# Optimization experiments

Measured on AMD Instinct MI355X. Metric: run time of the kernel, lower is better.

The kernel has to match this reference:

```python
import jax, jax.numpy as jnp
import numpy as np


def setup_inputs() -> dict:
    key = jax.random.key(0)
    k1, k2, k3, k4 = jax.random.split(key, 4)
    B, C, T, H, W = 2, 64, 8, 48, 48
    C2 = C // 2
    x_in = jax.random.normal(k1, (B, C, T, H, W), dtype=jnp.float32)
    # per-time-slice 1x1 conv weights (theta/phi pairs), kaiming-ish scale
    theta_w = jax.random.normal(k2, (T, C2, C), dtype=jnp.float32) / np.sqrt(C)
    phi_w = jax.random.normal(k3, (T, C2, C), dtype=jnp.float32) / np.sqrt(C)
    out_w = jax.random.normal(k4, (C, C), dtype=jnp.float32) / np.sqrt(C)
    return {"x_in": x_in, "theta_w": theta_w, "phi_w": phi_w, "out_w": out_w}


def reference(x_in, theta_w, phi_w, out_w):
    B, C, T, H, W = x_in.shape
    C2 = theta_w.shape[1]
    P = H * W
    # [B, T, C, P] layout: flatten spatial, move time next to batch
    x = jnp.transpose(x_in, (0, 2, 1, 3, 4)).reshape(B, T, C, P)
    # per-slice 1x1 convs == per-slice channel matmuls with slice-specific weights
    theta = jnp.einsum("toc,btcp->btop", theta_w, x)  # [B,T,C2,P]
    phi = jnp.einsum("toc,btcp->btop", phi_w, x)      # [B,T,C2,P]
    scale = 1.0 / jnp.sqrt(jnp.asarray(C2, dtype=x_in.dtype))
    scores = jnp.einsum("btcp,btcq->btpq", theta, phi) * scale  # [B,T,P,P]
    attn = jax.nn.softmax(scores, axis=-1)
    f = jnp.einsum("btpq,btcq->btcp", attn, x)  # value = raw x, [B,T,C,P]
    # conv_out: 1x1x1 Conv3d (pointwise over channels), then residual
    out = jnp.einsum("oc,btcp->btop", out_w, f)
    out = jnp.transpose(out.reshape(B, T, C, H, W), (0, 2, 1, 3, 4))
    return out + x_in
```

## Files before the change

kernel.cpp:

```cpp
#include <hip/hip_runtime.h>
#include <hip/hip_bf16.h>

#define CC 64
#define TT 8
#define PP 2304
#define C2 32
#define BT 16
#define NKT 36
#define HKT 18
#define SCALE2 0.25503486f

using h8 = __attribute__((ext_vector_type(8))) _Float16;
using h4 = __attribute__((ext_vector_type(4))) _Float16;
using f4 = __attribute__((ext_vector_type(4))) float;

#if __has_builtin(__builtin_amdgcn_exp2f)
#define EXP2(v) __builtin_amdgcn_exp2f(v)
#else
#define EXP2(v) exp2f(v)
#endif

#define SWIZ_BT(xcd, g) ((xcd) + 8 * ((g) & 1))
#define SWIZ_PT(g) ((g) >> 1)


__global__ __launch_bounds__(256) void k_prep(
    const float* __restrict__ x, const float* __restrict__ tw,
    const float* __restrict__ pw, _Float16* __restrict__ thf,
    _Float16* __restrict__ rec) {
  const int qt = SWIZ_PT(blockIdx.y), bt = SWIZ_BT(blockIdx.x, blockIdx.y);
  const int b = bt >> 3, t = bt & 7;
  const int tid = threadIdx.x;
  const int wv = tid >> 6, lane = tid & 63;
  const int quad = lane >> 4, l15 = lane & 15;

  __shared__ __align__(16) float x_s[64][68];
  __shared__ __align__(16) _Float16 th_s[4][16][32];
  __shared__ __align__(16) _Float16 ph_s[4][16][32];

  const size_t xslice = ((size_t)b * CC * TT + t) * PP;
  const int qg0 = qt * 64;

  {
    const int qq = tid & 63;
    const int c0 = (tid >> 6) * 16;
#pragma unroll
    for (int i = 0; i < 16; i++) {
      int c = c0 + i;
      x_s[qq][c] = x[xslice + (size_t)c * (TT * PP) + qg0 + qq];
    }
  }
  __syncthreads();

  h8 bx[2];
#pragma unroll
  for (int ks = 0; ks < 2; ks++) {
    const float* row = &x_s[wv * 16 + l15][ks * 32 + quad * 8];
    float4 u0 = *reinterpret_cast<const float4*>(row);
    float4 u1 = *reinterpret_cast<const float4*>(row + 4);
    bx[ks][0] = (_Float16)u0.x; bx[ks][1] = (_Float16)u0.y;
    bx[ks][2] = (_Float16)u0.z; bx[ks][3] = (_Float16)u0.w;
    bx[ks][4] = (_Float16)u1.x; bx[ks][5] = (_Float16)u1.y;
    bx[ks][6] = (_Float16)u1.z; bx[ks][7] = (_Float16)u1.w;
  }

  const float* twt = tw + t * C2 * CC;
  const float* pwt = pw + t * C2 * CC;
  const f4 zero = {0.f, 0.f, 0.f, 0.f};
  f4 accT[2] = {zero, zero}, accP[2] = {zero, zero};
#pragma unroll
  for (int mt = 0; mt < 2; mt++)
#pragma unroll
    for (int ks = 0; ks < 2; ks++) {
      const float* wr = twt + (mt * 16 + l15) * CC + ks * 32 + quad * 8;
      const float* pr = pwt + (mt * 16 + l15) * CC + ks * 32 + quad * 8;
      float4 a0 = *reinterpret_cast<const float4*>(wr);
      float4 a1 = *reinterpret_cast<const float4*>(wr + 4);
      float4 p0 = *reinterpret_cast<const float4*>(pr);
      float4 p1 = *reinterpret_cast<const float4*>(pr + 4);
      h8 at = {(_Float16)a0.x, (_Float16)a0.y, (_Float16)a0.z, (_Float16)a0.w,
               (_Float16)a1.x, (_Float16)a1.y, (_Float16)a1.z, (_Float16)a1.w};
      h8 ap = {(_Float16)p0.x, (_Float16)p0.y, (_Float16)p0.z, (_Float16)p0.w,
               (_Float16)p1.x, (_Float16)p1.y, (_Float16)p1.z, (_Float16)p1.w};
      accT[mt] =
          __builtin_amdgcn_mfma_f32_16x16x32_f16(at, bx[ks], accT[mt], 0, 0, 0);
      accP[mt] =
          __builtin_amdgcn_mfma_f32_16x16x32_f16(ap, bx[ks], accP[mt], 0, 0, 0);
    }

#pragma unroll
  for (int mt = 0; mt < 2; mt++) {
    h4 tv, pv;
#pragma unroll
    for (int r = 0; r < 4; r++) {
      tv[r] = (_Float16)(accT[mt][r] * SCALE2);
      pv[r] = (_Float16)accP[mt][r];
    }
    *reinterpret_cast<h4*>(&th_s[wv][l15][mt * 16 + quad * 4]) = tv;
    *reinterpret_cast<h4*>(&ph_s[wv][l15][mt * 16 + quad * 4]) = pv;
  }

  h8 tfrag = *reinterpret_cast<const h8*>(&th_s[wv][l15][quad * 8]);
  *reinterpret_cast<h8*>(
      thf + (((size_t)(bt * NKT + qt) * 4 + wv) * 64 + lane) * 8) = tfrag;

  _Float16* rb = rec + (size_t)(bt * NKT + qt) * 6144;
  h8 pfrag = *reinterpret_cast<const h8*>(&ph_s[wv][l15][quad * 8]);
  *reinterpret_cast<h8*>(rb + wv * 512 + lane * 8) = pfrag;

#pragma unroll
  for (int ctp = 0; ctp < 2; ctp++) {
    h8 v;
#pragma unroll
    for (int j = 0; j < 4; j++) {
      v[j] = (_Float16)x_s[wv * 16 + quad * 4 + j][(2 * ctp) * 16 + l15];
      v[4 + j] = (_Float16)x_s[wv * 16 + quad * 4 + j][(2 * ctp + 1) * 16 + l15];
    }
    *reinterpret_cast<h8*>(rb + 2048 + (wv * 2 + ctp) * 512 + lane * 8) = v;
  }
}

__global__ __launch_bounds__(512, 4) void k_attn(
    const float* __restrict__ x, const _Float16* __restrict__ thf,
    const _Float16* __restrict__ rec, const float* __restrict__ ow,
    float* __restrict__ out) {
  const int pt = SWIZ_PT(blockIdx.y), bt = SWIZ_BT(blockIdx.x, blockIdx.y);
  const int b = bt >> 3, t = bt & 7;
  const int tid = threadIdx.x;
  const int wv = tid >> 6, lane = tid & 63;
  const int quad = lane >> 4, l15 = lane & 15;
  const int qg = wv & 3, kg = wv >> 2;

  __shared__ __align__(16) char smem[49152];
  _Float16* stage = reinterpret_cast<_Float16*>(smem);
  float* exch = reinterpret_cast<float*>(smem);
  float* out_s = reinterpret_cast<float*>(smem + 20480);

  const h8 b_th = *reinterpret_cast<const h8*>(
      thf + (((size_t)(bt * NKT + pt) * 4 + qg) * 64 + lane) * 8);

  const _Float16* recb = rec + (size_t)bt * NKT * 6144;

  const int m0 = wv * 3;
  int ch_tile[3], ch_off[3];
#pragma unroll
  for (int j = 0; j < 3; j++) {
    int m = m0 + j;
    ch_tile[j] = m / 12;
    ch_off[j] = (m % 12) * 512 + lane * 8;
  }

  int4 v[3];
#pragma unroll
  for (int j = 0; j < 3; j++) {
    v[j] = *reinterpret_cast<const int4*>(recb +
                                          (size_t)(ch_tile[j] * HKT) * 6144 +
                                          ch_off[j]);
    *reinterpret_cast<int4*>(stage + ch_tile[j] * 6144 + ch_off[j]) = v[j];
  }

  const f4 zero = {0.f, 0.f, 0.f, 0.f};
  f4 O[4] = {zero, zero, zero, zero};
  float l_sum = 0.f;

  for (int i = 0; i < HKT; i++) {
    __syncthreads();
    const _Float16* cur = stage + (i & 1) * 12288 + kg * 6144;

    if (i < HKT - 1) {
#pragma unroll
      for (int j = 0; j < 3; j++)
        v[j] = *reinterpret_cast<const int4*>(
            recb + (size_t)(ch_tile[j] * HKT + i + 1) * 6144 + ch_off[j]);
    }

    h8 aphi[4];
#pragma unroll
    for (int nt = 0; nt < 4; nt++)
      aphi[nt] = *reinterpret_cast<const h8*>(cur + nt * 512 + lane * 8);
    f4 s[4];
#pragma unroll
    for (int nt = 0; nt < 4; nt++)
      s[nt] =
          __builtin_amdgcn_mfma_f32_16x16x32_f16(aphi[nt], b_th, zero, 0, 0, 0);

#pragma unroll
    for (int nt = 0; nt < 4; nt++) {
      h4 bw;
#pragma unroll
      for (int r = 0; r < 4; r++) {
        float w = EXP2(s[nt][r]);
        l_sum += w;
        bw[r] = (_Float16)w;
      }
#pragma unroll
      for (int ctp = 0; ctp < 2; ctp++) {
        h8 xx = *reinterpret_cast<const h8*>(cur + 2048 +
                                             (nt * 2 + ctp) * 512 + lane * 8);
        h4 a0 = __builtin_shufflevector(xx, xx, 0, 1, 2, 3);
        h4 a1 = __builtin_shufflevector(xx, xx, 4, 5, 6, 7);
        O[2 * ctp] =
            __builtin_amdgcn_mfma_f32_16x16x16f16(a0, bw, O[2 * ctp], 0, 0, 0);
        O[2 * ctp + 1] = __builtin_amdgcn_mfma_f32_16x16x16f16(
            a1, bw, O[2 * ctp + 1], 0, 0, 0);
      }
    }

    if (i < HKT - 1) {
#pragma unroll
      for (int j = 0; j < 3; j++)
        *reinterpret_cast<int4*>(stage + ((i + 1) & 1) * 12288 +
                                 ch_tile[j] * 6144 + ch_off[j]) = v[j];
    }
  }

  l_sum += __shfl_xor(l_sum, 16);
  l_sum += __shfl_xor(l_sum, 32);

  __syncthreads();

  if (kg == 1) {
#pragma unroll
    for (int k = 0; k < 16; k++)
      exch[(qg * 17 + k) * 64 + lane] = O[k >> 2][k & 3];
    exch[(qg * 17 + 16) * 64 + lane] = l_sum;
  }
  __syncthreads();

  if (kg == 0) {
#pragma unroll
    for (int k = 0; k < 16; k++)
      O[k >> 2][k & 3] += exch[(qg * 17 + k) * 64 + lane];
    const float inv = 1.f / (l_sum + exch[(qg * 17 + 16) * 64 + lane]);

    h4 bf[4];
#pragma unroll
    for (int ct = 0; ct < 4; ct++)
#pragma unroll
      for (int r = 0; r < 4; r++) bf[ct][r] = (_Float16)(O[ct][r] * inv);

    f4 D3[4] = {zero, zero, zero, zero};
#pragma unroll
    for (int mt = 0; mt < 4; mt++)
#pragma unroll
      for (int ct = 0; ct < 4; ct++) {
        const float* wrow =
            ow + (size_t)(mt * 16 + l15) * CC + ct * 16 + quad * 4;
        float4 u = *reinterpret_cast<const float4*>(wrow);
        h4 aw = {(_Float16)u.x, (_Float16)u.y, (_Float16)u.z, (_Float16)u.w};
        D3[mt] =
            __builtin_amdgcn_mfma_f32_16x16x16f16(aw, bf[ct], D3[mt], 0, 0, 0);
      }

#pragma unroll
    for (int mt = 0; mt < 4; mt++)
#pragma unroll
      for (int r = 0; r < 4; r++)
        out_s[(mt * 16 + quad * 4 + r) * 68 + qg * 16 + l15] = D3[mt][r];
  }
  __syncthreads();

  const int co = tid >> 3;
  const int psub = (tid & 7) * 8;
  const size_t gbase = ((size_t)(b * CC + co) * TT + t) * PP + pt * 64 + psub;
#pragma unroll
  for (int jj = 0; jj < 2; jj++) {
    float4 vo =
        *reinterpret_cast<const float4*>(&out_s[co * 68 + psub + jj * 4]);
    float4 xr = *reinterpret_cast<const float4*>(&x[gbase + jj * 4]);
    vo.x += xr.x; vo.y += xr.y; vo.z += xr.z; vo.w += xr.w;
    *reinterpret_cast<float4*>(&out[gbase + jj * 4]) = vo;
  }
}

extern "C" void kernel_launch(void* const* d_in, const int* in_sizes, int n_in,
                              void* d_out, int out_size, void* d_ws,
                              size_t ws_size, hipStream_t stream) {
  (void)in_sizes; (void)n_in; (void)out_size; (void)ws_size;
  const float* x = (const float*)d_in[0];
  const float* tw = (const float*)d_in[1];
  const float* pw = (const float*)d_in[2];
  const float* ow = (const float*)d_in[3];
  float* out = (float*)d_out;

  _Float16* thf = (_Float16*)d_ws;
  _Float16* rec = thf + (size_t)BT * NKT * 4 * 64 * 8;

  k_prep<<<dim3(8, 72), 256, 0, stream>>>(x, tw, pw, thf, rec);
  k_attn<<<dim3(8, 72), 512, 0, stream>>>(x, thf, rec, ow, out);
}
```

Baseline: 109.9 us.

## Restructure attention kernel to per-wave query strips with register double-buffered keys

The attention kernel moves from 512-thread blocks that split keys across two wave groups and share LDS staging to 128-thread blocks. In these, each wave owns two 16-query fragments and streams every key tile straight from global memory into registers with double buffering. This removes LDS staging, __syncthreads, and the cross-wave reduction of partial outputs. The PV step now uses 16x16x32 MFMAs on a re-laid-out value record produced by k_prep. In exchange, each wave reloads the full key/value records from global or L2, register pressure rises, and output stores become uncoalesced scalar writes.

```diff
diff --git a/kernel.cpp b/kernel.cpp
--- a/kernel.cpp
+++ b/kernel.cpp
@@ -7,7 +7,6 @@
 #define C2 32
 #define BT 16
 #define NKT 36
-#define HKT 18
 #define SCALE2 0.25503486f
 
 using h8 = __attribute__((ext_vector_type(8))) _Float16;
@@ -108,169 +107,138 @@
   h8 pfrag = *reinterpret_cast<const h8*>(&ph_s[wv][l15][quad * 8]);
   *reinterpret_cast<h8*>(rb + wv * 512 + lane * 8) = pfrag;
 
-#pragma unroll
-  for (int ctp = 0; ctp < 2; ctp++) {
-    h8 v;
-#pragma unroll
-    for (int j = 0; j < 4; j++) {
-      v[j] = (_Float16)x_s[wv * 16 + quad * 4 + j][(2 * ctp) * 16 + l15];
-      v[4 + j] = (_Float16)x_s[wv * 16 + quad * 4 + j][(2 * ctp + 1) * 16 + l15];
-    }
-    *reinterpret_cast<h8*>(rb + 2048 + (wv * 2 + ctp) * 512 + lane * 8) = v;
+  {
+    const int g = wv >> 1;
+#pragma unroll
+    for (int ct2 = 0; ct2 < 2; ct2++) {
+      const int ct = (wv & 1) * 2 + ct2;
+      h8 v;
+#pragma unroll
+      for (int j = 0; j < 4; j++) {
+        v[j] = (_Float16)x_s[32 * g + quad * 4 + j][ct * 16 + l15];
+        v[4 + j] = (_Float16)x_s[32 * g + 16 + quad * 4 + j][ct * 16 + l15];
+      }
+      *reinterpret_cast<h8*>(rb + 2048 + (g * 4 + ct) * 512 + lane * 8) = v;
+    }
   }
 }
 
-__global__ __launch_bounds__(512, 4) void k_attn(
+__global__ __launch_bounds__(128, 2) void k_attn(
     const float* __restrict__ x, const _Float16* __restrict__ thf,
     const _Float16* __restrict__ rec, const float* __restrict__ ow,
     float* __restrict__ out) {
-  const int pt = SWIZ_PT(blockIdx.y), bt = SWIZ_BT(blockIdx.x, blockIdx.y);
+  const int pb = SWIZ_PT(blockIdx.y);
+  const int bt = SWIZ_BT(blockIdx.x, blockIdx.y);
   const int b = bt >> 3, t = bt & 7;
   const int tid = threadIdx.x;
   const int wv = tid >> 6, lane = tid & 63;
   const int quad = lane >> 4, l15 = lane & 15;
-  const int qg = wv & 3, kg = wv >> 2;
-
-  __shared__ __align__(16) char smem[49152];
-  _Float16* stage = reinterpret_cast<_Float16*>(smem);
-  float* exch = reinterpret_cast<float*>(smem);
-  float* out_s = reinterpret_cast<float*>(smem + 20480);
-
-  const h8 b_th = *reinterpret_cast<const h8*>(
-      thf + (((size_t)(bt * NKT + pt) * 4 + qg) * 64 + lane) * 8);
-
-  const _Float16* recb = rec + (size_t)bt * NKT * 6144;
-
-  const int m0 = wv * 3;
-  int ch_tile[3], ch_off[3];
-#pragma unroll
-  for (int j = 0; j < 3; j++) {
-    int m = m0 + j;
-    ch_tile[j] = m / 12;
-    ch_off[j] = (m % 12) * 512 + lane * 8;
-  }
-
-  int4 v[3];
-#pragma unroll
-  for (int j = 0; j < 3; j++) {
-    v[j] = *reinterpret_cast<const int4*>(recb +
-                                          (size_t)(ch_tile[j] * HKT) * 6144 +
-                                          ch_off[j]);
-    *reinterpret_cast<int4*>(stage + ch_tile[j] * 6144 + ch_off[j]) = v[j];
-  }
+  const int pstrip = pb * 2 + wv;
+
+  const h8 bth0 = *reinterpret_cast<const h8*>(
+      thf + (((size_t)bt * 144 + pstrip * 2 + 0) * 64 + lane) * 8);
+  const h8 bth1 = *reinterpret_cast<const h8*>(
+      thf + (((size_t)bt * 144 + pstrip * 2 + 1) * 64 + lane) * 8);
+
+  const _Float16* recb = rec + (size_t)bt * NKT * 6144 + lane * 8;
 
   const f4 zero = {0.f, 0.f, 0.f, 0.f};
-  f4 O[4] = {zero, zero, zero, zero};
-  float l_sum = 0.f;
-
-  for (int i = 0; i < HKT; i++) {
-    __syncthreads();
-    const _Float16* cur = stage + (i & 1) * 12288 + kg * 6144;
-
-    if (i < HKT - 1) {
-#pragma unroll
-      for (int j = 0; j < 3; j++)
-        v[j] = *reinterpret_cast<const int4*>(
-            recb + (size_t)(ch_tile[j] * HKT + i + 1) * 6144 + ch_off[j]);
-    }
-
-    h8 aphi[4];
-#pragma unroll
-    for (int nt = 0; nt < 4; nt++)
-      aphi[nt] = *reinterpret_cast<const h8*>(cur + nt * 512 + lane * 8);
-    f4 s[4];
-#pragma unroll
-    for (int nt = 0; nt < 4; nt++)
-      s[nt] =
-          __builtin_amdgcn_mfma_f32_16x16x32_f16(aphi[nt], b_th, zero, 0, 0, 0);
-
-#pragma unroll
-    for (int nt = 0; nt < 4; nt++) {
-      h4 bw;
-#pragma unroll
-      for (int r = 0; r < 4; r++) {
-        float w = EXP2(s[nt][r]);
-        l_sum += w;
-        bw[r] = (_Float16)w;
-      }
-#pragma unroll
-      for (int ctp = 0; ctp < 2; ctp++) {
-        h8 xx = *reinterpret_cast<const h8*>(cur + 2048 +
-                                             (nt * 2 + ctp) * 512 + lane * 8);
-        h4 a0 = __builtin_shufflevector(xx, xx, 0, 1, 2, 3);
-        h4 a1 = __builtin_shufflevector(xx, xx, 4, 5, 6, 7);
-        O[2 * ctp] =
-            __builtin_amdgcn_mfma_f32_16x16x16f16(a0, bw, O[2 * ctp], 0, 0, 0);
-        O[2 * ctp + 1] = __builtin_amdgcn_mfma_f32_16x16x16f16(
-            a1, bw, O[2 * ctp + 1], 0, 0, 0);
-      }
-    }
-
-    if (i < HKT - 1) {
-#pragma unroll
-      for (int j = 0; j < 3; j++)
-        *reinterpret_cast<int4*>(stage + ((i + 1) & 1) * 12288 +
-                                 ch_tile[j] * 6144 + ch_off[j]) = v[j];
-    }
-  }
-
-  l_sum += __shfl_xor(l_sum, 16);
-  l_sum += __shfl_xor(l_sum, 32);
-
-  __syncthreads();
-
-  if (kg == 1) {
-#pragma unroll
-    for (int k = 0; k < 16; k++)
-      exch[(qg * 17 + k) * 64 + lane] = O[k >> 2][k & 3];
-    exch[(qg * 17 + 16) * 64 + lane] = l_sum;
-  }
-  __syncthreads();
-
-  if (kg == 0) {
-#pragma unroll
-    for (int k = 0; k < 16; k++)
-      O[k >> 2][k & 3] += exch[(qg * 17 + k) * 64 + lane];
-    const float inv = 1.f / (l_sum + exch[(qg * 17 + 16) * 64 + lane]);
-
-    h4 bf[4];
-#pragma unroll
-    for (int ct = 0; ct < 4; ct++)
-#pragma unroll
-      for (int r = 0; r < 4; r++) bf[ct][r] = (_Float16)(O[ct][r] * inv);
-
-    f4 D3[4] = {zero, zero, zero, zero};
-#pragma unroll
-    for (int mt = 0; mt < 4; mt++)
-#pragma unroll
-      for (int ct = 0; ct < 4; ct++) {
-        const float* wrow =
-            ow + (size_t)(mt * 16 + l15) * CC + ct * 16 + quad * 4;
-        float4 u = *reinterpret_cast<const float4*>(wrow);
-        h4 aw = {(_Float16)u.x, (_Float16)u.y, (_Float16)u.z, (_Float16)u.w};
-        D3[mt] =
-            __builtin_amdgcn_mfma_f32_16x16x16f16(aw, bf[ct], D3[mt], 0, 0, 0);
-      }
-
-#pragma unroll
-    for (int mt = 0; mt < 4; mt++)
-#pragma unroll
-      for (int r = 0; r < 4; r++)
-        out_s[(mt * 16 + quad * 4 + r) * 68 + qg * 16 + l15] = D3[mt][r];
-  }
-  __syncthreads();
-
-  const int co = tid >> 3;
-  const int psub = (tid & 7) * 8;
-  const size_t gbase = ((size_t)(b * CC + co) * TT + t) * PP + pt * 64 + psub;
-#pragma unroll
-  for (int jj = 0; jj < 2; jj++) {
-    float4 vo =
-        *reinterpret_cast<const float4*>(&out_s[co * 68 + psub + jj * 4]);
-    float4 xr = *reinterpret_cast<const float4*>(&x[gbase + jj * 4]);
-    vo.x += xr.x; vo.y += xr.y; vo.z += xr.z; vo.w += xr.w;
-    *reinterpret_cast<float4*>(&out[gbase + jj * 4]) = vo;
-  }
+  f4 O[4][2];
+#pragma unroll
+  for (int ct = 0; ct < 4; ct++) {
+    O[ct][0] = zero;
+    O[ct][1] = zero;
+  }
+  float lsum[2] = {0.f, 0.f};
+
+  h8 Abuf[12], Bbuf[12];
+
+#define LOADREC(BUF, kt)                                          \
+  {                                                               \
+    const _Float16* _p = recb + (size_t)(kt)*6144;                \
+    _Pragma("unroll") for (int j = 0; j < 12; j++)                \
+        BUF[j] = *reinterpret_cast<const h8*>(_p + j * 512);      \
+  }
+
+#define COMPUTE(BUF)                                                          \
+  {                                                                           \
+    f4 s[2][4];                                                               \
+    _Pragma("unroll") for (int pf = 0; pf < 2; pf++)                          \
+        _Pragma("unroll") for (int nt = 0; nt < 4; nt++)                      \
+            s[pf][nt] = __builtin_amdgcn_mfma_f32_16x16x32_f16(               \
+                BUF[nt], pf ? bth1 : bth0, zero, 0, 0, 0);                    \
+    _Pragma("unroll") for (int pf = 0; pf < 2; pf++)                          \
+        _Pragma("unroll") for (int g = 0; g < 2; g++) {                       \
+      h8 bw;                                                                  \
+      _Pragma("unroll") for (int r = 0; r < 4; r++) {                         \
+        float w0 = EXP2(s[pf][2 * g][r]);                                     \
+        float w1 = EXP2(s[pf][2 * g + 1][r]);                                 \
+        lsum[pf] += w0 + w1;                                                  \
+        bw[r] = (_Float16)w0;                                                 \
+        bw[4 + r] = (_Float16)w1;                                             \
+      }                                                                       \
+      _Pragma("unroll") for (int ct = 0; ct < 4; ct++)                        \
+          O[ct][pf] = __builtin_amdgcn_mfma_f32_16x16x32_f16(                 \
+              BUF[4 + g * 4 + ct], bw, O[ct][pf], 0, 0, 0);                   \
+    }                                                                         \
+  }
+
+  LOADREC(Abuf, 0);
+  for (int kt = 0; kt < NKT; kt += 2) {
+    LOADREC(Bbuf, kt + 1);
+    COMPUTE(Abuf);
+    if (kt + 2 < NKT) LOADREC(Abuf, kt + 2);
+    COMPUTE(Bbuf);
+  }
+#undef LOADREC
+#undef COMPUTE
+
+#pragma unroll
+  for (int pf = 0; pf < 2; pf++) {
+    lsum[pf] += __shfl_xor(lsum[pf], 16);
+    lsum[pf] += __shfl_xor(lsum[pf], 32);
+  }
+  const float inv0 = 1.f / lsum[0], inv1 = 1.f / lsum[1];
+
+  h4 bf[4][2];
+#pragma unroll
+  for (int ct = 0; ct < 4; ct++)
+#pragma unroll
+    for (int r = 0; r < 4; r++) {
+      bf[ct][0][r] = (_Float16)(O[ct][0][r] * inv0);
+      bf[ct][1][r] = (_Float16)(O[ct][1][r] * inv1);
+    }
+
+  f4 D3[4][2];
+#pragma unroll
+  for (int mt = 0; mt < 4; mt++) {
+    D3[mt][0] = zero;
+    D3[mt][1] = zero;
+  }
+#pragma unroll
+  for (int mt = 0; mt < 4; mt++)
+#pragma unroll
+    for (int ct = 0; ct < 4; ct++) {
+      const float* wrow =
+          ow + (size_t)(mt * 16 + l15) * CC + ct * 16 + quad * 4;
+      float4 u = *reinterpret_cast<const float4*>(wrow);
+      h4 aw = {(_Float16)u.x, (_Float16)u.y, (_Float16)u.z, (_Float16)u.w};
+      D3[mt][0] =
+          __builtin_amdgcn_mfma_f32_16x16x16f16(aw, bf[ct][0], D3[mt][0], 0, 0, 0);
+      D3[mt][1] =
+          __builtin_amdgcn_mfma_f32_16x16x16f16(aw, bf[ct][1], D3[mt][1], 0, 0, 0);
+    }
+
+  const int p0g = pstrip * 32 + l15;
+#pragma unroll
+  for (int mt = 0; mt < 4; mt++)
+#pragma unroll
+    for (int r = 0; r < 4; r++) {
+      const int o = mt * 16 + quad * 4 + r;
+      const size_t base = ((size_t)(b * CC + o) * TT + t) * PP + p0g;
+      out[base] = D3[mt][0][r] + x[base];
+      out[base + 16] = D3[mt][1][r] + x[base + 16];
+    }
 }
 
 extern "C" void kernel_launch(void* const* d_in, const int* in_sizes, int n_in,
@@ -287,5 +255,5 @@
   _Float16* rec = thf + (size_t)BT * NKT * 4 * 64 * 8;
 
   k_prep<<<dim3(8, 72), 256, 0, stream>>>(x, tw, pw, thf, rec);
-  k_attn<<<dim3(8, 72), 512, 0, stream>>>(x, thf, rec, ow, out);
+  k_attn<<<dim3(8, 72), 128, 0, stream>>>(x, thf, rec, ow, out);
 }
```

Result: faster. 106.9 us (-2.8%).
